# Performance work log

Hardware: AMD Instinct MI355X
Metric: run time of the kernel (lower is better)

The kernel has to match this reference:

```python
import jax, jax.numpy as jnp
import numpy as np

DIM = 2048
NH = 16
NKV = 4
HD = DIM // NH            # 128
KVD = HD * NKV            # 512
MLP = int(DIM * 4.0 * 2 / 3)  # 5461
EPS = 1.1920929e-07       # torch.finfo(float32).eps (nn.RMSNorm default)
ROPE_BASE = 10000.0


def act_quant(x):
    # per-token int8 absmax quantization (BitNet b1.58)
    scale = 127.0 / jnp.clip(jnp.max(jnp.abs(x), axis=-1, keepdims=True), 1e-5)
    return jnp.clip(jnp.round(x * scale), -128.0, 127.0) / scale


def weight_quant(w):
    # ternary weights via mean-absmax scale (BitNet b1.58)
    scale = 1.0 / jnp.clip(jnp.mean(jnp.abs(w)), 1e-5)
    return jnp.clip(jnp.round(w * scale), -1.0, 1.0) / scale


def bitlinear(x, w, b=None):
    # straight-through estimator quantization, then dense matmul
    xq = x + jax.lax.stop_gradient(act_quant(x) - x)
    wq = w + jax.lax.stop_gradient(weight_quant(w) - w)
    y = xq @ wq.T
    return y if b is None else y + b


def rmsnorm(x, w):
    return x * jax.lax.rsqrt(jnp.mean(x * x, axis=-1, keepdims=True) + EPS) * w


def rope_cos_sin(pos, head_dim, dtype):
    inv_freq = 1.0 / (ROPE_BASE ** (jnp.arange(0, head_dim, 2, dtype=jnp.float32) / head_dim))
    freqs = pos[..., None].astype(jnp.float32) * inv_freq  # [B,N,HD/2]
    cos = jnp.repeat(jnp.cos(freqs), 2, axis=-1).astype(dtype)  # interleaved [B,N,HD]
    sin = jnp.repeat(jnp.sin(freqs), 2, axis=-1).astype(dtype)
    return cos, sin


def rotate_interleave(x):
    x1 = x[..., 0::2]
    x2 = x[..., 1::2]
    return jnp.stack([-x2, x1], axis=-1).reshape(x.shape)


def apply_rope(x, cos, sin):
    # x: [B,H,N,HD]; cos/sin: [B,N,HD]
    return x * cos[:, None] + rotate_interleave(x) * sin[:, None]


def setup_inputs() -> dict:
    key = jax.random.key(0)
    ks = jax.random.split(key, 16)
    B, N = 2, 2048
    s = 0.02
    return {
        "x": jax.random.normal(ks[0], (B, N, DIM), jnp.float32),
        "position_ids": jnp.broadcast_to(jnp.arange(N, dtype=jnp.int32), (B, N)),
        "norm1_w": jnp.ones((DIM,), jnp.float32),
        "q_w": jax.random.normal(ks[1], (DIM, DIM), jnp.float32) * s,
        "q_b": jnp.zeros((DIM,), jnp.float32),
        "k_w": jax.random.normal(ks[2], (KVD, DIM), jnp.float32) * s,
        "k_b": jnp.zeros((KVD,), jnp.float32),
        "v_w": jax.random.normal(ks[3], (KVD, DIM), jnp.float32) * s,
        "v_b": jnp.zeros((KVD,), jnp.float32),
        "o_w": jax.random.normal(ks[4], (DIM, DIM), jnp.float32) * s,
        "norm2_w": jnp.ones((DIM,), jnp.float32),
        "gate_w": jax.random.normal(ks[5], (MLP, DIM), jnp.float32) * s,
        "up_w": jax.random.normal(ks[6], (MLP, DIM), jnp.float32) * s,
        "down_w": jax.random.normal(ks[7], (DIM, MLP), jnp.float32) * s,
    }


def reference(x, position_ids, norm1_w, q_w, q_b, k_w, k_b, v_w, v_b, o_w,
              norm2_w, gate_w, up_w, down_w):
    B, N, C = x.shape
    # --- attention ---
    h = rmsnorm(x, norm1_w)
    q = bitlinear(h, q_w, q_b).reshape(B, N, NH, HD).transpose(0, 2, 1, 3)
    k = bitlinear(h, k_w, k_b).reshape(B, N, NKV, HD).transpose(0, 2, 1, 3)
    v = bitlinear(h, v_w, v_b).reshape(B, N, NKV, HD).transpose(0, 2, 1, 3)
    cos, sin = rope_cos_sin(position_ids, HD, x.dtype)
    q = apply_rope(q, cos, sin)
    k = apply_rope(k, cos, sin)
    g = NH // NKV
    k = jnp.repeat(k, g, axis=1)  # GQA head expansion -> [B,NH,N,HD]
    v = jnp.repeat(v, g, axis=1)
    scores = jnp.einsum('bhqd,bhkd->bhqk', q, k) * (HD ** -0.5)
    causal_mask = jnp.triu(jnp.ones((N, N), bool), 1)
    scores = jnp.where(causal_mask, -jnp.inf, scores)
    attn = jax.nn.softmax(scores, axis=-1)
    out = jnp.einsum('bhqk,bhkd->bqhd', attn, v).reshape(B, N, C)
    x = x + bitlinear(out, o_w)
    # --- SwiGLU MLP ---
    h = rmsnorm(x, norm2_w)
    x = x + bitlinear(jax.nn.silu(bitlinear(h, gate_w)) * bitlinear(h, up_w), down_w)
    return x
```

## Files before the change

### kernel.cpp

```cpp
#include <hip/hip_runtime.h>

typedef unsigned short u16;
typedef unsigned int   u32;
typedef unsigned char  u8;

using bf16x8 = __attribute__((ext_vector_type(8))) short;
using f32x4  = __attribute__((ext_vector_type(4))) float;
using i32x4  = __attribute__((ext_vector_type(4))) int;

#define SEQ    2048
#define DIMC   2048
#define TOK    4096
#define QKV_N  3072
#define GU_N   11008
#define MLP_P  5504
#define MLP_R  5461
#define ATT_SCALE 0.08838834764831845f

__device__ __forceinline__ float bf2f(u16 v){ return __uint_as_float(((u32)v) << 16); }
__device__ __forceinline__ u16 f2bf(float f){
  u32 x = __float_as_uint(f);
  u32 r = (x + 0x7fffu + ((x >> 16) & 1u)) >> 16;
  return (u16)r;
}

__device__ __forceinline__ float waveRedSum(float v){
#pragma unroll
  for (int o = 32; o > 0; o >>= 1) v += __shfl_xor(v, o);
  return v;
}
__device__ __forceinline__ float waveRedMax(float v){
#pragma unroll
  for (int o = 32; o > 0; o >>= 1) v = fmaxf(v, __shfl_xor(v, o));
  return v;
}

#define GLD16(gp, lp) __builtin_amdgcn_global_load_lds( \
    (__attribute__((address_space(1))) void*)(gp), \
    (__attribute__((address_space(3))) void*)(lp), 16, 0, 0)

__global__ __launch_bounds__(256) void k_abssum7(
    const float4* __restrict__ w0, const float4* __restrict__ w1,
    const float4* __restrict__ w2, const float4* __restrict__ w3,
    const float4* __restrict__ w4, const float4* __restrict__ w5,
    const float4* __restrict__ w6, float* __restrict__ sc){
  const int rg = blockIdx.y;
  const float4* w = rg==0?w0: rg==1?w1: rg==2?w2: rg==3?w3: rg==4?w4: rg==5?w5: w6;
  const int n4 = (rg==0||rg==3) ? 1048576 : (rg<4 ? 262144 : 2796032);
  float s = 0.f;
  for (int i = blockIdx.x*256 + threadIdx.x; i < n4; i += gridDim.x*256){
    float4 v = w[i];
    s += fabsf(v.x) + fabsf(v.y) + fabsf(v.z) + fabsf(v.w);
  }
  s = waveRedSum(s);
  __shared__ float sm[4];
  int lane = threadIdx.x & 63, wv = threadIdx.x >> 6;
  if (lane == 0) sm[wv] = s;
  __syncthreads();
  if (threadIdx.x == 0) atomicAdd(sc + rg, sm[0]+sm[1]+sm[2]+sm[3]);
}

__global__ void k_finalize(float* __restrict__ sc){
  if (threadIdx.x == 0){
    const float counts[7] = {4194304.f, 1048576.f, 1048576.f, 4194304.f,
                             11184128.f, 11184128.f, 11184128.f};
    for (int i = 0; i < 7; i++) sc[8+i] = fmaxf(sc[i]/counts[i], 1e-5f);
  }
}

__global__ __launch_bounds__(256) void k_wquant6(
    const float4* __restrict__ w0, const float4* __restrict__ w1,
    const float4* __restrict__ w2, const float4* __restrict__ w3,
    const float4* __restrict__ w4, const float4* __restrict__ w5,
    u32* __restrict__ d0, u32* __restrict__ d1, u32* __restrict__ d2,
    u32* __restrict__ d3, u32* __restrict__ d4, u32* __restrict__ d5,
    const float* __restrict__ sc){
  const int rg = blockIdx.y;
  const float4* src = rg==0?w0: rg==1?w1: rg==2?w2: rg==3?w3: rg==4?w4: w5;
  u32* dst = rg==0?d0: rg==1?d1: rg==2?d2: rg==3?d3: rg==4?d4: d5;
  const int n4 = (rg==0||rg==3) ? 1048576 : (rg<4 ? 262144 : 2796032);
  float ws = 1.0f / sc[8+rg];
  for (int i = blockIdx.x*256 + threadIdx.x; i < n4; i += gridDim.x*256){
    float4 v = src[i];
    int c0 = (int)fminf(fmaxf(rintf(v.x*ws), -1.f), 1.f);
    int c1 = (int)fminf(fmaxf(rintf(v.y*ws), -1.f), 1.f);
    int c2 = (int)fminf(fmaxf(rintf(v.z*ws), -1.f), 1.f);
    int c3 = (int)fminf(fmaxf(rintf(v.w*ws), -1.f), 1.f);
    dst[i] = (u32)(u8)c0 | ((u32)(u8)c1 << 8) | ((u32)(u8)c2 << 16) | ((u32)(u8)c3 << 24);
  }
}

__global__ __launch_bounds__(256) void k_wquant_down(const float* __restrict__ src,
                                                     u32* __restrict__ dst,
                                                     const float* __restrict__ deqp){
  int i = blockIdx.x*256 + threadIdx.x;
  const int total = 2048*(MLP_P/4);
  if (i >= total) return;
  float ws = 1.0f / deqp[0];
  int r = i / (MLP_P/4);
  int c4 = (i - r*(MLP_P/4))*4;
  u32 o = 0;
#pragma unroll
  for (int e = 0; e < 4; e++){
    int c = c4 + e;
    int t = 0;
    if (c < MLP_R) t = (int)fminf(fmaxf(rintf(src[(long)r*MLP_R + c]*ws), -1.f), 1.f);
    o |= (u32)(u8)t << (8*e);
  }
  dst[i] = o;
}

__global__ __launch_bounds__(256) void k_rmsq(const float* __restrict__ in,
                                              const float* __restrict__ nw,
                                              char* __restrict__ outq,
                                              float* __restrict__ rowdeq, int do_norm){
  const int row = blockIdx.x, tid = threadIdx.x;
  const float* xp = in + (long)row * DIMC + tid*8;
  float v[8];
  float4 a0 = *(const float4*)xp;
  float4 a1 = *(const float4*)(xp + 4);
  v[0]=a0.x; v[1]=a0.y; v[2]=a0.z; v[3]=a0.w;
  v[4]=a1.x; v[5]=a1.y; v[6]=a1.z; v[7]=a1.w;
  float ss = 0.f;
#pragma unroll
  for (int j = 0; j < 8; j++) ss += v[j]*v[j];
  __shared__ float sm[8];
  int lane = tid & 63, wv = tid >> 6;
  ss = waveRedSum(ss);
  if (lane == 0) sm[wv] = ss;
  __syncthreads();
  float h[8];
  float amax = 0.f;
  if (do_norm){
    float tot = sm[0]+sm[1]+sm[2]+sm[3];
    float rms = rsqrtf(tot * (1.0f/DIMC) + 1.1920929e-07f);
    float4 w0 = *(const float4*)(nw + tid*8);
    float4 w1 = *(const float4*)(nw + tid*8 + 4);
    float wr8[8] = {w0.x,w0.y,w0.z,w0.w,w1.x,w1.y,w1.z,w1.w};
#pragma unroll
    for (int j = 0; j < 8; j++){ h[j] = v[j]*rms*wr8[j]; amax = fmaxf(amax, fabsf(h[j])); }
  } else {
#pragma unroll
    for (int j = 0; j < 8; j++){ h[j] = v[j]; amax = fmaxf(amax, fabsf(h[j])); }
  }
  amax = waveRedMax(amax);
  if (lane == 0) sm[4+wv] = amax;
  __syncthreads();
  float gmax = fmaxf(fmaxf(sm[4],sm[5]), fmaxf(sm[6],sm[7]));
  float sc = 127.0f / fmaxf(gmax, 1e-5f);
  int2 o;
  char* oc = (char*)&o;
#pragma unroll
  for (int j = 0; j < 8; j++)
    oc[j] = (char)(int)fminf(fmaxf(rintf(h[j]*sc), -128.f), 127.f);
  *(int2*)(outq + (long)row*DIMC + tid*8) = o;
  if (tid == 0) rowdeq[row] = 1.0f / sc;
}

__global__ __launch_bounds__(256) void k_ropevt(u16* __restrict__ y,
                                                const int* __restrict__ pos_ids,
                                                u16* __restrict__ VT){
  if (blockIdx.x < 20480){
    int idx = blockIdx.x*256 + threadIdx.x;
    int m = idx / 1280;
    int p = idx - m*1280;
    int c = p*2;
    int i = (c & 127) >> 1;
    float pos = (float)pos_ids[m];
    float inv = expf((float)i * -0.14391156831212787f);
    float f = pos * inv;
    float sn, cs;
    sincosf(f, &sn, &cs);
    u32* pr = (u32*)(y + (long)m*QKV_N + c);
    u32 both = *pr;
    float x0 = bf2f((u16)(both & 0xffffu));
    float x1 = bf2f((u16)(both >> 16));
    u16 o0 = f2bf(x0*cs - x1*sn);
    u16 o1 = f2bf(x1*cs + x0*sn);
    *pr = (u32)o0 | ((u32)o1 << 16);
  } else {
    int idx = (blockIdx.x - 20480)*256 + threadIdx.x;
    int d  = idx & 127;
    int hk = (idx >> 7) & 3;
    int b  = (idx >> 9) & 1;
    int tg = idx >> 10;
    int tok0 = tg*8;
    const u16* src = y + ((long)b*SEQ + tok0)*QKV_N + 2560 + hk*128 + d;
    u16 tmp[8];
#pragma unroll
    for (int e = 0; e < 8; e++) tmp[e] = src[(long)e*QKV_N];
    *(int4*)(VT + (((long)(b*4+hk))*128 + d)*SEQ + tok0) = *(int4*)tmp;
  }
}

template<int MODE>
__global__ __launch_bounds__(256) void k_gemm(
    const char* __restrict__ A, const char* __restrict__ B,
    int K, int lda, int ldb, int ldc,
    const float* __restrict__ rowdeq, const float* __restrict__ deqp,
    const float* __restrict__ bq, const float* __restrict__ bk, const float* __restrict__ bv,
    const float* __restrict__ resid, float* __restrict__ outF, u16* __restrict__ outB)
{
  __shared__ char sA[128*64];
  __shared__ char sB[128*64];
  const int tid = threadIdx.x;
  const int lane = tid & 63, wv = tid >> 6;
  const int wr = wv >> 1, wc = wv & 1;
  const long m0 = (long)blockIdx.y * 128;
  const long n0 = (long)blockIdx.x * 128;
  const int r = lane & 15, qq = lane >> 4;

  i32x4 acc[4][4];
#pragma unroll
  for (int i = 0; i < 4; i++)
#pragma unroll
    for (int j = 0; j < 4; j++) acc[i][j] = (i32x4){0,0,0,0};

  const int c0 = tid, c1 = tid + 256;
  const char* gA0 = A + (m0 + (c0>>2))*lda + (c0&3)*16;
  const char* gA1 = A + (m0 + (c1>>2))*lda + (c1&3)*16;
  const char* gB0 = B + (n0 + (c0>>2))*ldb + (c0&3)*16;
  const char* gB1 = B + (n0 + (c1>>2))*ldb + (c1&3)*16;
  char* lA0 = sA + c0*16; char* lA1 = sA + c1*16;
  char* lB0 = sB + c0*16; char* lB1 = sB + c1*16;

  GLD16(gA0, lA0);
  GLD16(gA1, lA1);
  GLD16(gB0, lB0);
  GLD16(gB1, lB1);
  __syncthreads();

  for (int kt = 0; kt < K; kt += 64){
    i32x4 aF[4], bF[4];
#pragma unroll
    for (int i = 0; i < 4; i++) aF[i] = *(const i32x4*)(sA + (wr*64 + 16*i + r)*64 + qq*16);
#pragma unroll
    for (int j = 0; j < 4; j++) bF[j] = *(const i32x4*)(sB + (wc*64 + 16*j + r)*64 + qq*16);
    __syncthreads();
    if (kt + 64 < K){
      GLD16(gA0 + kt + 64, lA0);
      GLD16(gA1 + kt + 64, lA1);
      GLD16(gB0 + kt + 64, lB0);
      GLD16(gB1 + kt + 64, lB1);
    }
#pragma unroll
    for (int i = 0; i < 4; i++)
#pragma unroll
      for (int j = 0; j < 4; j++)
        acc[i][j] = __builtin_amdgcn_mfma_i32_16x16x64_i8(aF[i], bF[j], acc[i][j], 0, 0, 0);
    __syncthreads();
  }

#pragma unroll
  for (int i = 0; i < 4; i++){
#pragma unroll
    for (int t = 0; t < 4; t++){
      const long row = m0 + wr*64 + 16*i + 4*qq + t;
      const float rdv = rowdeq[row];
#pragma unroll
      for (int j = 0; j < 4; j++){
        const long col = n0 + wc*64 + 16*j + r;
        float vv = (float)acc[i][j][t];
        if (MODE == 0){
          int sec = (col >= 2048) + (col >= 2560);
          float dq = deqp[sec];
          float bias = (sec == 0) ? bq[col] : (sec == 1) ? bk[col-2048] : bv[col-2560];
          outB[row*(long)ldc + col] = f2bf(vv*rdv*dq + bias);
        } else if (MODE == 1){
          outF[row*(long)ldc + col] = vv*rdv*deqp[0] + resid[row*(long)ldc + col];
        } else {
          int sec = (col >= 5504) ? 1 : 0;
          outB[row*(long)ldc + col] = f2bf(vv*rdv*deqp[sec]);
        }
      }
    }
  }
}

__global__ __launch_bounds__(256) void k_attn(const u16* __restrict__ Y,
                                              const u16* __restrict__ VT,
                                              float* __restrict__ O)
{
  __shared__ u16 Ks[64*128];
  __shared__ u16 VTs[128*64];
  __shared__ u16 Ps[64][72];

  const int pp = blockIdx.x;
  const int bh = blockIdx.y;
  const int b = bh >> 4, h = bh & 15, hk = h >> 2;
  const int tid = threadIdx.x;
  const int lane = tid & 63, wv = tid >> 6;
  const int r = lane & 15, qq = lane >> 4;
  const long rowbase = (long)b * SEQ;
  const u16* Kbase = Y + rowbase*QKV_N + 2048 + hk*128;
  const u16* Vbase = VT + ((long)(b*4+hk))*128*SEQ;

  for (int ph = 0; ph < 2; ph++){
    const int qt = ph ? pp : 31 - pp;
    const int q0 = qt * 64;

    bf16x8 qf[4];
#pragma unroll
    for (int kc = 0; kc < 4; kc++)
      qf[kc] = *(const bf16x8*)(Y + (rowbase + q0 + wv*16 + r)*QKV_N + h*128 + kc*32 + qq*8);

#pragma unroll
    for (int rnd = 0; rnd < 4; rnd++){
      int c = rnd*256 + tid;
      int row = c >> 4, g = (c & 15) ^ (row & 7);
      GLD16(Kbase + ((long)(qt*0 + row))*QKV_N + g*8, (char*)Ks + c*16);
    }
#pragma unroll
    for (int rnd = 0; rnd < 4; rnd++){
      int c = rnd*256 + tid;
      int d = c >> 3, g = (c & 7) ^ (d & 7);
      GLD16(Vbase + (long)d*SEQ + g*8, (char*)VTs + c*16);
    }
    __syncthreads();

    f32x4 accO[8];
#pragma unroll
    for (int jn = 0; jn < 8; jn++) accO[jn] = (f32x4){0.f,0.f,0.f,0.f};
    float m_run[4] = {-INFINITY,-INFINITY,-INFINITY,-INFINITY};
    float l_run[4] = {0.f,0.f,0.f,0.f};

    for (int kt = 0; kt <= qt; kt++){
      float sv[4][4];
#pragma unroll
      for (int j = 0; j < 4; j++){
        f32x4 a = (f32x4){0.f,0.f,0.f,0.f};
#pragma unroll
        for (int kc = 0; kc < 4; kc++){
          bf16x8 kf = *(const bf16x8*)(Ks + (16*j + r)*128 + (((kc*4 + qq) ^ (r & 7)))*8);
          a = __builtin_amdgcn_mfma_f32_16x16x32_bf16(qf[kc], kf, a, 0, 0, 0);
        }
#pragma unroll
        for (int t = 0; t < 4; t++) sv[j][t] = a[t] * ATT_SCALE;
      }
      __syncthreads();
      if (kt < qt){
#pragma unroll
        for (int rnd = 0; rnd < 4; rnd++){
          int c = rnd*256 + tid;
          int row = c >> 4, g = (c & 15) ^ (row & 7);
          GLD16(Kbase + ((long)((kt+1)*64 + row))*QKV_N + g*8, (char*)Ks + c*16);
        }
      }
      if (kt == qt){
#pragma unroll
        for (int j = 0; j < 4; j++){
          int key = kt*64 + 16*j + r;
#pragma unroll
          for (int t = 0; t < 4; t++){
            int qr = q0 + wv*16 + 4*qq + t;
            if (key > qr) sv[j][t] = -INFINITY;
          }
        }
      }
#pragma unroll
      for (int t = 0; t < 4; t++){
        float mm = fmaxf(fmaxf(sv[0][t],sv[1][t]), fmaxf(sv[2][t],sv[3][t]));
#pragma unroll
        for (int o = 8; o > 0; o >>= 1) mm = fmaxf(mm, __shfl_xor(mm, o));
        float mnew = fmaxf(m_run[t], mm);
        float alpha = __expf(m_run[t] - mnew);
        m_run[t] = mnew;
        float ps = 0.f;
#pragma unroll
        for (int j = 0; j < 4; j++){
          float p = __expf(sv[j][t] - mnew);
          ps += p;
          Ps[wv*16 + 4*qq + t][16*j + r] = f2bf(p);
        }
#pragma unroll
        for (int o = 8; o > 0; o >>= 1) ps += __shfl_xor(ps, o);
        l_run[t] = l_run[t]*alpha + ps;
#pragma unroll
        for (int jn = 0; jn < 8; jn++) accO[jn][t] *= alpha;
      }
#pragma unroll
      for (int kc = 0; kc < 2; kc++){
        bf16x8 pf = *(const bf16x8*)&Ps[wv*16 + r][kc*32 + qq*8];
#pragma unroll
        for (int jn = 0; jn < 8; jn++){
          bf16x8 vf = *(const bf16x8*)(VTs + (16*jn + r)*64 + (((kc*4 + qq) ^ (r & 7)))*8);
          accO[jn] = __builtin_amdgcn_mfma_f32_16x16x32_bf16(pf, vf, accO[jn], 0, 0, 0);
        }
      }
      __syncthreads();
      if (kt < qt){
#pragma unroll
        for (int rnd = 0; rnd < 4; rnd++){
          int c = rnd*256 + tid;
          int d = c >> 3, g = (c & 7) ^ (d & 7);
          GLD16(Vbase + (long)d*SEQ + (kt+1)*64 + g*8, (char*)VTs + c*16);
        }
      }
    }
    float inv[4];
#pragma unroll
    for (int t = 0; t < 4; t++) inv[t] = 1.0f / l_run[t];
#pragma unroll
    for (int jn = 0; jn < 8; jn++){
#pragma unroll
      for (int t = 0; t < 4; t++){
        long row = rowbase + q0 + wv*16 + 4*qq + t;
        O[row*DIMC + h*128 + 16*jn + r] = accO[jn][t]*inv[t];
      }
    }
    __syncthreads();
  }
}

__global__ __launch_bounds__(256) void k_swiglu(const u16* __restrict__ ygu,
                                                char* __restrict__ qout,
                                                float* __restrict__ rowdeq){
  const int row = blockIdx.x, tid = threadIdx.x;
  const u16* base = ygu + (long)row * GU_N;
  float h[24];
  float amax = 0.f;
#pragma unroll
  for (int it = 0; it < 3; it++){
    int chunk = it*256 + tid;
    if (chunk < 688){
      int j0 = chunk*8;
      int4 g4 = *(const int4*)(base + j0);
      int4 u4 = *(const int4*)(base + MLP_P + j0);
      const u16* gp = (const u16*)&g4;
      const u16* up = (const u16*)&u4;
#pragma unroll
      for (int e = 0; e < 8; e++){
        float g = bf2f(gp[e]);
        float u = bf2f(up[e]);
        float hv = g * (1.0f/(1.0f + __expf(-g))) * u;
        h[it*8+e] = hv;
        amax = fmaxf(amax, fabsf(hv));
      }
    } else {
#pragma unroll
      for (int e = 0; e < 8; e++) h[it*8+e] = 0.f;
    }
  }
  amax = waveRedMax(amax);
  __shared__ float sm[4];
  int lane = tid & 63, wv = tid >> 6;
  if (lane == 0) sm[wv] = amax;
  __syncthreads();
  float gmax = fmaxf(fmaxf(sm[0],sm[1]), fmaxf(sm[2],sm[3]));
  float sc = 127.0f / fmaxf(gmax, 1e-5f);
#pragma unroll
  for (int it = 0; it < 3; it++){
    int chunk = it*256 + tid;
    if (chunk < 688){
      int j0 = chunk*8;
      int2 o;
      char* oc = (char*)&o;
#pragma unroll
      for (int e = 0; e < 8; e++)
        oc[e] = (char)(int)fminf(fmaxf(rintf(h[it*8+e]*sc), -128.f), 127.f);
      *(int2*)(qout + (long)row*MLP_P + j0) = o;
    }
  }
  if (tid == 0) rowdeq[row] = 1.0f/sc;
}

extern "C" void kernel_launch(void* const* d_in, const int* in_sizes, int n_in,
                              void* d_out, int out_size, void* d_ws, size_t ws_size,
                              hipStream_t stream)
{
  (void)in_sizes; (void)n_in; (void)out_size; (void)ws_size;
  const float* x   = (const float*)d_in[0];
  const int*   pos = (const int*)d_in[1];
  const float* n1w = (const float*)d_in[2];
  const float* qw  = (const float*)d_in[3];
  const float* qb  = (const float*)d_in[4];
  const float* kw  = (const float*)d_in[5];
  const float* kb  = (const float*)d_in[6];
  const float* vw  = (const float*)d_in[7];
  const float* vb  = (const float*)d_in[8];
  const float* ow  = (const float*)d_in[9];
  const float* n2w = (const float*)d_in[10];
  const float* gw  = (const float*)d_in[11];
  const float* uw  = (const float*)d_in[12];
  const float* dw  = (const float*)d_in[13];
  float* out = (float*)d_out;
  char* ws = (char*)d_ws;

  float* sc   = (float*)ws;
  char* Wqkv  = ws + 256;
  char* Wo    = ws + 6291712;
  char* Wgu   = ws + 10486016;
  char* Wd    = ws + 33030400;
  char* actq  = ws + 44302592;
  char* swq   = ws + 52691200;
  float* rd   = (float*)(ws + 75235584);
  char* xreg  = ws + 75252224;
  u16* yqkv   = (u16*)xreg;
  float* attn = (float*)(xreg + 25165824);
  u16* vT     = (u16*)(xreg + 58720256);
  u16* ygu    = (u16*)xreg;

  hipMemsetAsync(sc, 0, 64, stream);
  k_abssum7<<<dim3(512,7),256,0,stream>>>((const float4*)qw, (const float4*)kw,
                                          (const float4*)vw, (const float4*)ow,
                                          (const float4*)gw, (const float4*)uw,
                                          (const float4*)dw, sc);
  k_finalize<<<1,64,0,stream>>>(sc);
  k_wquant6<<<dim3(512,6),256,0,stream>>>((const float4*)qw, (const float4*)kw,
                                          (const float4*)vw, (const float4*)ow,
                                          (const float4*)gw, (const float4*)uw,
                                          (u32*)Wqkv, (u32*)(Wqkv + 2048l*2048),
                                          (u32*)(Wqkv + 2560l*2048), (u32*)Wo,
                                          (u32*)Wgu, (u32*)(Wgu + 5504l*2048), sc);
  hipMemsetAsync(Wgu + 5461l*2048,        0, 43l*2048, stream);
  hipMemsetAsync(Wgu + (5504l+5461)*2048, 0, 43l*2048, stream);
  k_wquant_down<<<11008,256,0,stream>>>(dw, (u32*)Wd, sc+14);

  k_rmsq<<<4096,256,0,stream>>>(x, n1w, actq, rd, 1);
  k_gemm<0><<<dim3(24,32),256,0,stream>>>(actq, Wqkv, 2048, 2048, 2048, 3072,
                                          rd, sc+8, qb, kb, vb, nullptr, nullptr, yqkv);
  k_ropevt<<<21504,256,0,stream>>>(yqkv, pos, vT);
  k_attn<<<dim3(16,32),256,0,stream>>>(yqkv, vT, attn);
  k_rmsq<<<4096,256,0,stream>>>(attn, n1w, actq, rd, 0);
  k_gemm<1><<<dim3(16,32),256,0,stream>>>(actq, Wo, 2048, 2048, 2048, 2048,
                                          rd, sc+11, nullptr, nullptr, nullptr, x, out, nullptr);

  k_rmsq<<<4096,256,0,stream>>>(out, n2w, actq, rd, 1);
  k_gemm<2><<<dim3(86,32),256,0,stream>>>(actq, Wgu, 2048, 2048, 2048, 11008,
                                          rd, sc+12, nullptr, nullptr, nullptr, nullptr, nullptr, ygu);
  k_swiglu<<<4096,256,0,stream>>>(ygu, swq, rd);
  k_gemm<1><<<dim3(16,32),256,0,stream>>>(swq, Wd, 5504, 5504, 5504, 2048,
                                          rd, sc+14, nullptr, nullptr, nullptr, out, out, nullptr);
}
```

Measured before the change: 726.5 us.

## Replace int8 GEMM with 512-thread double-buffered, swizzled, larger-tile kernel

Replaces the 128x128 single-buffer int8 MFMA GEMM with a templated 512-thread kernel using 256x128 or 256x256 tiles. Each K step of 128 is split into half-steps, and global-to-LDS loads for later stages are double-buffered and issued between MFMA phases, with explicit vmcnt waits and raw barriers. It also adds an XOR swizzle on the LDS layout to reduce bank conflicts, a grid-index swizzle for L2 locality, and s_setprio around the MFMA blocks. The large dynamic LDS use (up to 128KB) lowers occupancy, and the hand-written waitcnt and barrier scheme is fragile.

```diff
diff --git a/kernel.cpp b/kernel.cpp
--- a/kernel.cpp
+++ b/kernel.cpp
@@ -38,6 +38,10 @@
 #define GLD16(gp, lp) __builtin_amdgcn_global_load_lds( \
     (__attribute__((address_space(1))) void*)(gp), \
     (__attribute__((address_space(3))) void*)(lp), 16, 0, 0)
+
+#define FENCE() asm volatile("" ::: "memory")
+#define SBAR()  do{ FENCE(); __builtin_amdgcn_s_barrier(); FENCE(); }while(0)
+#define VMCNT(n) asm volatile("s_waitcnt vmcnt(" #n ")" ::: "memory")
 
 __global__ __launch_bounds__(256) void k_abssum7(
     const float4* __restrict__ w0, const float4* __restrict__ w1,
@@ -193,80 +197,168 @@
   }
 }
 
-template<int MODE>
-__global__ __launch_bounds__(256) void k_gemm(
+template<int BM, int BN, int WM, int WN, int MODE>
+__global__ __launch_bounds__(512, 2) void k_gemm8(
     const char* __restrict__ A, const char* __restrict__ B,
-    int K, int lda, int ldb, int ldc,
+    int K, int lda, int ldb, int ldc, int ntn,
     const float* __restrict__ rowdeq, const float* __restrict__ deqp,
     const float* __restrict__ bq, const float* __restrict__ bk, const float* __restrict__ bv,
     const float* __restrict__ resid, float* __restrict__ outF, u16* __restrict__ outB)
 {
-  __shared__ char sA[128*64];
-  __shared__ char sB[128*64];
+  constexpr int SM = BM/WM, SN = BN/WN;
+  constexpr int MR = SM/16, NR = SN/16, MRH = MR/2;
+  constexpr int RA = BM/128, RB = BN/128;
+  constexpr int ASZ = BM*64, BSZ = BN*64;
+  constexpr int BUFSZ = 2*(ASZ+BSZ);
+  extern __shared__ __align__(16) char sm8[];
+
   const int tid = threadIdx.x;
   const int lane = tid & 63, wv = tid >> 6;
-  const int wr = wv >> 1, wc = wv & 1;
-  const long m0 = (long)blockIdx.y * 128;
-  const long n0 = (long)blockIdx.x * 128;
+  const int wr = wv / WN, wc = wv % WN;
   const int r = lane & 15, qq = lane >> 4;
 
-  i32x4 acc[4][4];
-#pragma unroll
-  for (int i = 0; i < 4; i++)
-#pragma unroll
-    for (int j = 0; j < 4; j++) acc[i][j] = (i32x4){0,0,0,0};
-
-  const int c0 = tid, c1 = tid + 256;
-  const char* gA0 = A + (m0 + (c0>>2))*lda + (c0&3)*16;
-  const char* gA1 = A + (m0 + (c1>>2))*lda + (c1&3)*16;
-  const char* gB0 = B + (n0 + (c0>>2))*ldb + (c0&3)*16;
-  const char* gB1 = B + (n0 + (c1>>2))*ldb + (c1&3)*16;
-  char* lA0 = sA + c0*16; char* lA1 = sA + c1*16;
-  char* lB0 = sB + c0*16; char* lB1 = sB + c1*16;
-
-  GLD16(gA0, lA0);
-  GLD16(gA1, lA1);
-  GLD16(gB0, lB0);
-  GLD16(gB1, lB1);
-  __syncthreads();
-
-  for (int kt = 0; kt < K; kt += 64){
-    i32x4 aF[4], bF[4];
-#pragma unroll
-    for (int i = 0; i < 4; i++) aF[i] = *(const i32x4*)(sA + (wr*64 + 16*i + r)*64 + qq*16);
-#pragma unroll
-    for (int j = 0; j < 4; j++) bF[j] = *(const i32x4*)(sB + (wc*64 + 16*j + r)*64 + qq*16);
-    __syncthreads();
-    if (kt + 64 < K){
-      GLD16(gA0 + kt + 64, lA0);
-      GLD16(gA1 + kt + 64, lA1);
-      GLD16(gB0 + kt + 64, lB0);
-      GLD16(gB1 + kt + 64, lB1);
-    }
-#pragma unroll
-    for (int i = 0; i < 4; i++)
-#pragma unroll
-      for (int j = 0; j < 4; j++)
-        acc[i][j] = __builtin_amdgcn_mfma_i32_16x16x64_i8(aF[i], bF[j], acc[i][j], 0, 0, 0);
-    __syncthreads();
-  }
-
-#pragma unroll
-  for (int i = 0; i < 4; i++){
-#pragma unroll
-    for (int t = 0; t < 4; t++){
-      const long row = m0 + wr*64 + 16*i + 4*qq + t;
+  const int nwg = gridDim.x;
+  const int chunk = nwg >> 3;
+  const int lin = blockIdx.x;
+  const int swz = (lin & 7)*chunk + (lin >> 3);
+  const int mt = swz / ntn, nt = swz - mt*ntn;
+  const long m0 = (long)mt*BM, n0 = (long)nt*BN;
+
+  const char* __restrict__ gA = A + m0*lda;
+  const char* __restrict__ gB = B + n0*ldb;
+
+  int  soA[RA], soB[RB];
+  long goA[RA], goB[RB];
+#pragma unroll
+  for (int u = 0; u < RA; u++){
+    int c = u*512 + tid, row = c >> 2, gp = c & 3, g = gp ^ ((row>>1)&3);
+    soA[u] = c*16; goA[u] = (long)row*lda + g*16;
+  }
+#pragma unroll
+  for (int u = 0; u < RB; u++){
+    int c = u*512 + tid, row = c >> 2, gp = c & 3, g = gp ^ ((row>>1)&3);
+    soB[u] = c*16; goB[u] = (long)row*ldb + g*16;
+  }
+  const int gsw = (qq ^ ((r>>1)&3))*16;
+  const int aoff0 = (wr*SM + r)*64 + gsw;
+  const int boff0 = (wc*SN + r)*64 + gsw;
+
+  const int NT = K >> 7;
+
+  i32x4 acc[MR][NR];
+#pragma unroll
+  for (int i = 0; i < MR; i++)
+#pragma unroll
+    for (int j = 0; j < NR; j++) acc[i][j] = (i32x4){0,0,0,0};
+
+  auto stA = [&](int tq, int kh){
+    char* dst = sm8 + (tq&1)*BUFSZ + kh*ASZ;
+    const char* src = gA + (long)tq*128 + kh*64;
+#pragma unroll
+    for (int u = 0; u < RA; u++) GLD16(src + goA[u], dst + soA[u]);
+  };
+  auto stB = [&](int tq, int kh){
+    char* dst = sm8 + (tq&1)*BUFSZ + 2*ASZ + kh*BSZ;
+    const char* src = gB + (long)tq*128 + kh*64;
+#pragma unroll
+    for (int u = 0; u < RB; u++) GLD16(src + goB[u], dst + soB[u]);
+  };
+
+  stA(0,0); stB(0,0); stA(0,1); stB(0,1);
+  stA(1,0); stB(1,0);
+  if constexpr (RA+RB == 4) VMCNT(4); else VMCNT(3);
+  SBAR();
+
+  for (int t = 0; t < NT; t++){
+    const char* cA = sm8 + (t&1)*BUFSZ;
+    const char* cB = cA + 2*ASZ;
+    i32x4 bF[NR];
+    {
+      i32x4 aF[MRH];
+#pragma unroll
+      for (int i = 0; i < MRH; i++) aF[i] = *(const i32x4*)(cA + aoff0 + i*1024);
+#pragma unroll
+      for (int j = 0; j < NR; j++)  bF[j] = *(const i32x4*)(cB + boff0 + j*1024);
+      if (t+1 < NT) stA(t+1, 1);
+      SBAR();
+      __builtin_amdgcn_s_setprio(1);
+#pragma unroll
+      for (int i = 0; i < MRH; i++)
+#pragma unroll
+        for (int j = 0; j < NR; j++)
+          acc[i][j] = __builtin_amdgcn_mfma_i32_16x16x64_i8(aF[i], bF[j], acc[i][j], 0,0,0);
+      __builtin_amdgcn_s_setprio(0);
+      SBAR();
+    }
+    {
+      i32x4 aF[MRH];
+#pragma unroll
+      for (int i = 0; i < MRH; i++) aF[i] = *(const i32x4*)(cA + aoff0 + (MRH+i)*1024);
+      if (t+1 < NT) stB(t+1, 1);
+      SBAR();
+      __builtin_amdgcn_s_setprio(1);
+#pragma unroll
+      for (int i = 0; i < MRH; i++)
+#pragma unroll
+        for (int j = 0; j < NR; j++)
+          acc[MRH+i][j] = __builtin_amdgcn_mfma_i32_16x16x64_i8(aF[i], bF[j], acc[MRH+i][j], 0,0,0);
+      __builtin_amdgcn_s_setprio(0);
+      SBAR();
+    }
+    {
+      i32x4 aF[MRH];
+#pragma unroll
+      for (int i = 0; i < MRH; i++) aF[i] = *(const i32x4*)(cA + ASZ + aoff0 + i*1024);
+#pragma unroll
+      for (int j = 0; j < NR; j++)  bF[j] = *(const i32x4*)(cB + BSZ + boff0 + j*1024);
+      if (t+2 < NT) stA(t+2, 0);
+      SBAR();
+      __builtin_amdgcn_s_setprio(1);
+#pragma unroll
+      for (int i = 0; i < MRH; i++)
+#pragma unroll
+        for (int j = 0; j < NR; j++)
+          acc[i][j] = __builtin_amdgcn_mfma_i32_16x16x64_i8(aF[i], bF[j], acc[i][j], 0,0,0);
+      __builtin_amdgcn_s_setprio(0);
+      SBAR();
+    }
+    {
+      i32x4 aF[MRH];
+#pragma unroll
+      for (int i = 0; i < MRH; i++) aF[i] = *(const i32x4*)(cA + ASZ + aoff0 + (MRH+i)*1024);
+      if (t+2 < NT) stB(t+2, 0);
+      SBAR();
+      __builtin_amdgcn_s_setprio(1);
+#pragma unroll
+      for (int i = 0; i < MRH; i++)
+#pragma unroll
+        for (int j = 0; j < NR; j++)
+          acc[MRH+i][j] = __builtin_amdgcn_mfma_i32_16x16x64_i8(aF[i], bF[j], acc[MRH+i][j], 0,0,0);
+      __builtin_amdgcn_s_setprio(0);
+      if (t + 1 < NT){
+        if (t + 2 < NT){ if constexpr (RA+RB == 4) VMCNT(4); else VMCNT(3); }
+        else VMCNT(0);
+      }
+      SBAR();
+    }
+  }
+
+#pragma unroll
+  for (int i = 0; i < MR; i++){
+#pragma unroll
+    for (int tt = 0; tt < 4; tt++){
+      const long row = m0 + wr*SM + 16*i + 4*qq + tt;
       const float rdv = rowdeq[row];
 #pragma unroll
-      for (int j = 0; j < 4; j++){
-        const long col = n0 + wc*64 + 16*j + r;
-        float vv = (float)acc[i][j][t];
-        if (MODE == 0){
+      for (int j = 0; j < NR; j++){
+        const long col = n0 + wc*SN + 16*j + r;
+        float vv = (float)acc[i][j][tt];
+        if constexpr (MODE == 0){
           int sec = (col >= 2048) + (col >= 2560);
           float dq = deqp[sec];
           float bias = (sec == 0) ? bq[col] : (sec == 1) ? bk[col-2048] : bv[col-2560];
           outB[row*(long)ldc + col] = f2bf(vv*rdv*dq + bias);
-        } else if (MODE == 1){
+        } else if constexpr (MODE == 1){
           outF[row*(long)ldc + col] = vv*rdv*deqp[0] + resid[row*(long)ldc + col];
         } else {
           int sec = (col >= 5504) ? 1 : 0;
@@ -486,6 +578,17 @@
   float* out = (float*)d_out;
   char* ws = (char*)d_ws;
 
+  static int attr_done = 0;
+  if (!attr_done){
+    hipFuncSetAttribute(reinterpret_cast<const void*>(k_gemm8<256,128,4,2,0>),
+                        hipFuncAttributeMaxDynamicSharedMemorySize, 98304);
+    hipFuncSetAttribute(reinterpret_cast<const void*>(k_gemm8<256,128,4,2,1>),
+                        hipFuncAttributeMaxDynamicSharedMemorySize, 98304);
+    hipFuncSetAttribute(reinterpret_cast<const void*>(k_gemm8<256,256,2,4,2>),
+                        hipFuncAttributeMaxDynamicSharedMemorySize, 131072);
+    attr_done = 1;
+  }
+
   float* sc   = (float*)ws;
   char* Wqkv  = ws + 256;
   char* Wo    = ws + 6291712;
@@ -517,18 +620,18 @@
   k_wquant_down<<<11008,256,0,stream>>>(dw, (u32*)Wd, sc+14);
 
   k_rmsq<<<4096,256,0,stream>>>(x, n1w, actq, rd, 1);
-  k_gemm<0><<<dim3(24,32),256,0,stream>>>(actq, Wqkv, 2048, 2048, 2048, 3072,
+  k_gemm8<256,128,4,2,0><<<384,512,98304,stream>>>(actq, Wqkv, 2048, 2048, 2048, 3072, 24,
                                           rd, sc+8, qb, kb, vb, nullptr, nullptr, yqkv);
   k_ropevt<<<21504,256,0,stream>>>(yqkv, pos, vT);
   k_attn<<<dim3(16,32),256,0,stream>>>(yqkv, vT, attn);
   k_rmsq<<<4096,256,0,stream>>>(attn, n1w, actq, rd, 0);
-  k_gemm<1><<<dim3(16,32),256,0,stream>>>(actq, Wo, 2048, 2048, 2048, 2048,
+  k_gemm8<256,128,4,2,1><<<256,512,98304,stream>>>(actq, Wo, 2048, 2048, 2048, 2048, 16,
                                           rd, sc+11, nullptr, nullptr, nullptr, x, out, nullptr);
 
   k_rmsq<<<4096,256,0,stream>>>(out, n2w, actq, rd, 1);
-  k_gemm<2><<<dim3(86,32),256,0,stream>>>(actq, Wgu, 2048, 2048, 2048, 11008,
+  k_gemm8<256,256,2,4,2><<<688,512,131072,stream>>>(actq, Wgu, 2048, 2048, 2048, 11008, 43,
                                           rd, sc+12, nullptr, nullptr, nullptr, nullptr, nullptr, ygu);
   k_swiglu<<<4096,256,0,stream>>>(ygu, swq, rd);
-  k_gemm<1><<<dim3(16,32),256,0,stream>>>(swq, Wd, 5504, 5504, 5504, 2048,
+  k_gemm8<256,128,4,2,1><<<256,512,98304,stream>>>(swq, Wd, 5504, 5504, 5504, 2048, 16,
                                           rd, sc+14, nullptr, nullptr, nullptr, out, out, nullptr);
 }
```

Measured after the change: 684.3 us. 1.06x faster.
